# Kernel optimization log

Hardware: AMD Instinct MI355X
Metric: run time of the kernel (lower is better)

The kernel has to match this reference:

```python
import jax, jax.numpy as jnp
import numpy as np
from jax import lax

B, T, D = 4, 4096, 1024
NEG_BIG = -1e30  # stand-in for -inf initial max-state; identical after clamp(min=-30)


def setup_inputs() -> dict:
    key = jax.random.key(0)
    ks = jax.random.split(key, 10)
    x = jax.random.normal(ks[0], (B, T, D), dtype=jnp.float32)
    time_mix_k = jax.random.uniform(ks[1], (D,), dtype=jnp.float32)
    time_mix_v = jax.random.uniform(ks[2], (D,), dtype=jnp.float32)
    time_mix_r = jax.random.uniform(ks[3], (D,), dtype=jnp.float32)
    s = 1.0 / np.sqrt(D)
    W_k = jax.random.normal(ks[4], (D, D), dtype=jnp.float32) * s
    W_v = jax.random.normal(ks[5], (D, D), dtype=jnp.float32) * s
    W_r = jax.random.normal(ks[6], (D, D), dtype=jnp.float32) * s
    W_o = jax.random.normal(ks[7], (D, D), dtype=jnp.float32) * s
    time_decay = -(jax.random.uniform(ks[8], (D,), dtype=jnp.float32) + 0.5)
    time_first = jax.random.normal(ks[9], (D,), dtype=jnp.float32) * 0.1
    return {"x": x, "time_mix_k": time_mix_k, "time_mix_v": time_mix_v,
            "time_mix_r": time_mix_r, "W_k": W_k, "W_v": W_v, "W_r": W_r,
            "W_o": W_o, "time_decay": time_decay, "time_first": time_first}


def _wkv_scan(k, v, w, u):
    # k, v: [B, T, D]; w, u: [D]. Numerically-stable max-subtract WKV scan.
    b, t, d = k.shape
    p0 = jnp.full((b, d), NEG_BIG, dtype=k.dtype)  # running max exponent
    q0 = jnp.zeros((b, d), dtype=k.dtype)          # rescaled numerator state

    def step(carry, kv_t):
        p, q = carry
        k_t, v_t = kv_t
        new_p = jnp.maximum(p, u + k_t)
        scale_old = jnp.exp(jnp.maximum(p - new_p, -30.0))
        scale_cur = jnp.exp(jnp.maximum(u + k_t - new_p, -30.0))
        wkv = (scale_old * q + scale_cur * v_t) / (scale_old + scale_cur + 1e-9)
        new_p2 = jnp.maximum(p + w, k_t)
        scale_prev = jnp.exp(jnp.maximum(p + w - new_p2, -30.0))
        scale_new = jnp.exp(jnp.maximum(k_t - new_p2, -30.0))
        q2 = scale_prev * q + scale_new * v_t
        return (new_p2, q2), wkv

    kT = jnp.swapaxes(k, 0, 1)  # [T, B, D]
    vT = jnp.swapaxes(v, 0, 1)
    _, wkv = lax.scan(step, (p0, q0), (kT, vT))
    return jnp.swapaxes(wkv, 0, 1)  # [B, T, D]


def reference(x, time_mix_k, time_mix_v, time_mix_r, W_k, W_v, W_r, W_o,
              time_decay, time_first):
    # token shift: x_prev[t] = x[t-1], zeros at t=0
    x_prev = jnp.pad(x[:, :-1, :], ((0, 0), (1, 0), (0, 0)))
    xk = x * time_mix_k + x_prev * (1.0 - time_mix_k)
    xv = x * time_mix_v + x_prev * (1.0 - time_mix_v)
    xr = x * time_mix_r + x_prev * (1.0 - time_mix_r)
    # torch nn.Linear (no bias): y = x @ W.T
    k = jnp.einsum('btd,ed->bte', xk, W_k)
    v = jnp.einsum('btd,ed->bte', xv, W_v)
    r = jax.nn.sigmoid(jnp.einsum('btd,ed->bte', xr, W_r))
    wkv = _wkv_scan(k, v, time_decay, time_first)
    y = r * wkv
    return jnp.einsum('btd,ed->bte', y, W_o)
```

## Files before the change

kernel.cpp:

```cpp
#include <hip/hip_runtime.h>
#include <stdint.h>

#define D_DIM 1024
#define T_DIM 4096
#define B_DIM 4
#define M_DIM (B_DIM * T_DIM)
#define NCH 64
#define CHL 64
#define GEMM_N 1024
#define GEMM_K 1024

typedef short bf16x8 __attribute__((ext_vector_type(8)));
typedef float f32x4 __attribute__((ext_vector_type(4)));

__device__ __forceinline__ ushort f2bf(float f) {
    union { float f; uint32_t u; } x; x.f = f;
    uint32_t r = x.u + 0x7fffu + ((x.u >> 16) & 1u);
    return (ushort)(r >> 16);
}
__device__ __forceinline__ float bf2f(ushort u) {
    union { uint32_t u; float f; } x; x.u = (uint32_t)u << 16; return x.f;
}

__device__ __forceinline__ void gload16(const ushort* g, ushort* l) {
    __builtin_amdgcn_global_load_lds(
        (const __attribute__((address_space(1))) void*)g,
        (__attribute__((address_space(3))) void*)l, 16, 0, 0);
}

__global__ void convw(const float* __restrict__ w0, const float* __restrict__ w1,
                      const float* __restrict__ w2, const float* __restrict__ w3,
                      ushort* __restrict__ out) {
    int i = blockIdx.x * 256 + threadIdx.x;
    int sel = i >> 18;
    const float* src = sel == 0 ? w0 : sel == 1 ? w1 : sel == 2 ? w2 : w3;
    int off = (i & 0x3ffff) << 2;
    float4 f = *(const float4*)(src + off);
    ushort4 o; o.x = f2bf(f.x); o.y = f2bf(f.y); o.z = f2bf(f.z); o.w = f2bf(f.w);
    *(ushort4*)(out + (size_t)i * 4) = o;
}

__global__ void mixz(const float* __restrict__ x, const float* __restrict__ tm,
                     ushort* __restrict__ o) {
    size_t gid = (size_t)blockIdx.x * 256 + threadIdx.x;
    size_t e = gid * 4;
    int d = (int)(e & (D_DIM - 1));
    int t = (int)((e >> 10) & (T_DIM - 1));
    float4 xc = *(const float4*)(x + e);
    float4 xp = make_float4(0.f, 0.f, 0.f, 0.f);
    if (t > 0) xp = *(const float4*)(x + e - D_DIM);
    float4 m = *(const float4*)(tm + d);
    ushort4 r;
    r.x = f2bf(xc.x * m.x + xp.x * (1.f - m.x));
    r.y = f2bf(xc.y * m.y + xp.y * (1.f - m.y));
    r.z = f2bf(xc.z * m.z + xp.z * (1.f - m.z));
    r.w = f2bf(xc.w * m.w + xp.w * (1.f - m.w));
    *(ushort4*)(o + e) = r;
}

__global__ void mixall(const float* __restrict__ x,
                       const float* __restrict__ mk, const float* __restrict__ mv,
                       const float* __restrict__ mr,
                       ushort* __restrict__ xk, ushort* __restrict__ xv,
                       ushort* __restrict__ xr) {
    size_t gid = (size_t)blockIdx.x * 256 + threadIdx.x;
    size_t e = gid * 4;
    int d = (int)(e & (D_DIM - 1));
    int t = (int)((e >> 10) & (T_DIM - 1));
    float4 xc = *(const float4*)(x + e);
    float4 xp = make_float4(0.f, 0.f, 0.f, 0.f);
    if (t > 0) xp = *(const float4*)(x + e - D_DIM);
    float4 a = *(const float4*)(mk + d);
    float4 b = *(const float4*)(mv + d);
    float4 c = *(const float4*)(mr + d);
    ushort4 ok, ov, orr;
    ok.x = f2bf(xc.x * a.x + xp.x * (1.f - a.x));
    ok.y = f2bf(xc.y * a.y + xp.y * (1.f - a.y));
    ok.z = f2bf(xc.z * a.z + xp.z * (1.f - a.z));
    ok.w = f2bf(xc.w * a.w + xp.w * (1.f - a.w));
    ov.x = f2bf(xc.x * b.x + xp.x * (1.f - b.x));
    ov.y = f2bf(xc.y * b.y + xp.y * (1.f - b.y));
    ov.z = f2bf(xc.z * b.z + xp.z * (1.f - b.z));
    ov.w = f2bf(xc.w * b.w + xp.w * (1.f - b.w));
    orr.x = f2bf(xc.x * c.x + xp.x * (1.f - c.x));
    orr.y = f2bf(xc.y * c.y + xp.y * (1.f - c.y));
    orr.z = f2bf(xc.z * c.z + xp.z * (1.f - c.z));
    orr.w = f2bf(xc.w * c.w + xp.w * (1.f - c.w));
    *(ushort4*)(xk + e) = ok;
    *(ushort4*)(xv + e) = ov;
    *(ushort4*)(xr + e) = orr;
}

template <int OUTF32>
__global__ void __launch_bounds__(256)
gemm_bt(const ushort* __restrict__ A0, const ushort* __restrict__ B0,
        void* __restrict__ Cv, size_t sA, size_t sB, size_t sC) {
    constexpr int K = GEMM_K, N = GEMM_N;
    __shared__ ushort As[128 * 32];
    __shared__ ushort Bs[128 * 32];
    const int z = blockIdx.z;
    const ushort* A = A0 + (size_t)z * sA;
    const ushort* Bw = B0 + (size_t)z * sB;

    const int id = blockIdx.y * 8 + blockIdx.x;
    const int L = (id & 7) * 128 + (id >> 3);
    const int bx = L & 7, by = L >> 3;

    const int tid = threadIdx.x;
    const int wid = tid >> 6, lane = tid & 63;
    const int wr = wid >> 1, wc = wid & 1;

    const ushort* Ab = A + (size_t)by * 128 * K;
    const ushort* Bb = Bw + (size_t)bx * 128 * K;
    const ushort* ga = Ab + (size_t)(tid >> 2) * K + ((tid & 3) << 3);
    const ushort* gb = Bb + (size_t)(tid >> 2) * K + ((tid & 3) << 3);
    ushort* lA0 = &As[wid * 512];
    ushort* lA1 = &As[2048 + wid * 512];
    ushort* lB0 = &Bs[wid * 512];
    ushort* lB1 = &Bs[2048 + wid * 512];
    const size_t rstep = (size_t)64 * K;

    f32x4 acc[4][4] = {};
    const int frow = lane & 15;
    const int kgrp = (lane >> 4) << 3;

    for (int kt = 0; kt < K; kt += 32) {
        __syncthreads();
        gload16(ga + kt, lA0);
        gload16(ga + kt + rstep, lA1);
        gload16(gb + kt, lB0);
        gload16(gb + kt + rstep, lB1);
        __syncthreads();
        bf16x8 af[4], bfr[4];
#pragma unroll
        for (int m = 0; m < 4; ++m)
            af[m] = *(const bf16x8*)&As[(wr * 64 + m * 16 + frow) * 32 + kgrp];
#pragma unroll
        for (int n = 0; n < 4; ++n)
            bfr[n] = *(const bf16x8*)&Bs[(wc * 64 + n * 16 + frow) * 32 + kgrp];
#pragma unroll
        for (int m = 0; m < 4; ++m)
#pragma unroll
            for (int n = 0; n < 4; ++n)
                acc[m][n] = __builtin_amdgcn_mfma_f32_16x16x32_bf16(
                    af[m], bfr[n], acc[m][n], 0, 0, 0);
    }

    const int rsub = (lane >> 4) << 2;
    if (OUTF32) {
        float* C = (float*)Cv + (size_t)z * sC;
        const int col = bx * 128 + wc * 64 + frow;
        const int row0 = by * 128 + wr * 64 + rsub;
#pragma unroll
        for (int m = 0; m < 4; ++m)
#pragma unroll
            for (int n = 0; n < 4; ++n)
#pragma unroll
                for (int r = 0; r < 4; ++r)
                    C[(size_t)(row0 + m * 16 + r) * N + col + n * 16] = acc[m][n][r];
    } else {
        ushort* C = (ushort*)Cv + (size_t)z * sC;
        ushort* Cs = As;
        const int gRow0 = by * 128, gCol0 = bx * 128;
#pragma unroll
        for (int ch = 0; ch < 4; ++ch) {
            __syncthreads();
            if ((ch >> 1) == wr) {
                const int mb = (ch & 1) << 1;
#pragma unroll
                for (int mm = 0; mm < 2; ++mm)
#pragma unroll
                    for (int n = 0; n < 4; ++n)
#pragma unroll
                        for (int r = 0; r < 4; ++r) {
                            int lr = ((mb + mm) & 1) * 16 + rsub + r;
                            int lc = wc * 64 + n * 16 + frow;
                            Cs[lr * 128 + lc] = f2bf(acc[mb + mm][n][r]);
                        }
            }
            __syncthreads();
            const int lr1 = tid >> 4, lc1 = (tid & 15) << 3;
            size_t g1 = (size_t)(gRow0 + ch * 32 + lr1) * N + gCol0 + lc1;
            size_t g2 = (size_t)(gRow0 + ch * 32 + 16 + lr1) * N + gCol0 + lc1;
            *(bf16x8*)(C + g1) = *(const bf16x8*)&Cs[tid << 3];
            *(bf16x8*)(C + g2) = *(const bf16x8*)&Cs[2048 + (tid << 3)];
        }
    }
}

__global__ void wkv_passA4(const ushort* __restrict__ k, const ushort* __restrict__ v,
                           const float* __restrict__ w_, float* __restrict__ m_arr,
                           float* __restrict__ s_arr) {
    int gid = blockIdx.x * 256 + threadIdx.x;
    int d4 = gid & 255;
    int b = (gid >> 8) & 3;
    int c = gid >> 10;
    float4 w4 = *(const float4*)(w_ + d4 * 4);
    size_t base = ((size_t)(b * T_DIM + c * CHL)) * D_DIM + d4 * 4;
    float m0 = -1e30f, m1 = -1e30f, m2 = -1e30f, m3 = -1e30f;
    float s0 = 0.f, s1 = 0.f, s2 = 0.f, s3 = 0.f;
#pragma unroll 2
    for (int i = 0; i < CHL; ++i) {
        ushort4 k4 = *(const ushort4*)(k + base + (size_t)i * D_DIM);
        ushort4 v4 = *(const ushort4*)(v + base + (size_t)i * D_DIM);
        float cw = (float)(CHL - 1 - i);
        float e0 = bf2f(k4.x) + cw * w4.x, e1 = bf2f(k4.y) + cw * w4.y;
        float e2 = bf2f(k4.z) + cw * w4.z, e3 = bf2f(k4.w) + cw * w4.w;
        float n0 = fmaxf(m0, e0), n1 = fmaxf(m1, e1);
        float n2 = fmaxf(m2, e2), n3 = fmaxf(m3, e3);
        s0 = s0 * __expf(fmaxf(m0 - n0, -30.f)) + __expf(fmaxf(e0 - n0, -30.f)) * bf2f(v4.x);
        s1 = s1 * __expf(fmaxf(m1 - n1, -30.f)) + __expf(fmaxf(e1 - n1, -30.f)) * bf2f(v4.y);
        s2 = s2 * __expf(fmaxf(m2 - n2, -30.f)) + __expf(fmaxf(e2 - n2, -30.f)) * bf2f(v4.z);
        s3 = s3 * __expf(fmaxf(m3 - n3, -30.f)) + __expf(fmaxf(e3 - n3, -30.f)) * bf2f(v4.w);
        m0 = n0; m1 = n1; m2 = n2; m3 = n3;
    }
    int idx = ((c * B_DIM + b) << 10) + d4 * 4;
    *(float4*)(m_arr + idx) = make_float4(m0, m1, m2, m3);
    *(float4*)(s_arr + idx) = make_float4(s0, s1, s2, s3);
}

__global__ void wkv_passB(const float* __restrict__ m_arr, const float* __restrict__ s_arr,
                          const float* __restrict__ w_, float* __restrict__ pin,
                          float* __restrict__ qin) {
    int gid = blockIdx.x * 256 + threadIdx.x;
    int d = gid & 1023;
    int b = gid >> 10;
    float w = w_[d];
    float Lw = (float)CHL * w;
    float p = -1e30f, q = 0.f;
    for (int c = 0; c < NCH; ++c) {
        int idx = ((c * B_DIM + b) << 10) | d;
        pin[idx] = p; qin[idx] = q;
        float mc = m_arr[idx], sc = s_arr[idx];
        float pn = fmaxf(p + Lw, mc);
        q = __expf(fmaxf(p + Lw - pn, -30.f)) * q +
            __expf(fmaxf(mc - pn, -30.f)) * sc;
        p = pn;
    }
}

__global__ void wkv_passC4(const ushort* __restrict__ k, const ushort* __restrict__ v,
                           const ushort* __restrict__ r, const float* __restrict__ w_,
                           const float* __restrict__ u_, const float* __restrict__ pin,
                           const float* __restrict__ qin, ushort* __restrict__ y) {
    int gid = blockIdx.x * 256 + threadIdx.x;
    int d4 = gid & 255;
    int b = (gid >> 8) & 3;
    int c = gid >> 10;
    float4 w4 = *(const float4*)(w_ + d4 * 4);
    float4 u4 = *(const float4*)(u_ + d4 * 4);
    int sidx = ((c * B_DIM + b) << 10) + d4 * 4;
    float4 p4 = *(const float4*)(pin + sidx);
    float4 q4 = *(const float4*)(qin + sidx);
    float p0 = p4.x, p1 = p4.y, p2 = p4.z, p3 = p4.w;
    float q0 = q4.x, q1 = q4.y, q2 = q4.z, q3 = q4.w;
    size_t base = ((size_t)(b * T_DIM + c * CHL)) * D_DIM + d4 * 4;
#pragma unroll 2
    for (int i = 0; i < CHL; ++i) {
        ushort4 k4 = *(const ushort4*)(k + base);
        ushort4 v4 = *(const ushort4*)(v + base);
        ushort4 r4 = *(const ushort4*)(r + base);
        ushort4 o;
#define WKV_CH(P, Q, KK, VV, RR, W, U, OUT)                                   \
        {                                                                     \
            float kk = bf2f(KK), vv = bf2f(VV), rr = bf2f(RR);                \
            float uk = (U) + kk;                                              \
            float np = fmaxf(P, uk);                                          \
            float so = __expf(fmaxf(P - np, -30.f));                          \
            float sc = __expf(fmaxf(uk - np, -30.f));                         \
            float wkv = (so * Q + sc * vv) / (so + sc + 1e-9f);               \
            float np2 = fmaxf(P + (W), kk);                                   \
            float sp = __expf(fmaxf(P + (W) - np2, -30.f));                   \
            float sn = __expf(fmaxf(kk - np2, -30.f));                        \
            Q = sp * Q + sn * vv;                                             \
            P = np2;                                                          \
            float sig = 1.f / (1.f + __expf(-rr));                            \
            OUT = f2bf(sig * wkv);                                            \
        }
        WKV_CH(p0, q0, k4.x, v4.x, r4.x, w4.x, u4.x, o.x)
        WKV_CH(p1, q1, k4.y, v4.y, r4.y, w4.y, u4.y, o.y)
        WKV_CH(p2, q2, k4.z, v4.z, r4.z, w4.z, u4.z, o.z)
        WKV_CH(p3, q3, k4.w, v4.w, r4.w, w4.w, u4.w, o.w)
#undef WKV_CH
        *(ushort4*)(y + base) = o;
        base += D_DIM;
    }
}

extern "C" void kernel_launch(void* const* d_in, const int* in_sizes, int n_in,
                              void* d_out, int out_size, void* d_ws, size_t ws_size,
                              hipStream_t stream) {
    (void)in_sizes; (void)n_in; (void)out_size;
    const float* x  = (const float*)d_in[0];
    const float* mk = (const float*)d_in[1];
    const float* mv = (const float*)d_in[2];
    const float* mr = (const float*)d_in[3];
    const float* Wk = (const float*)d_in[4];
    const float* Wv = (const float*)d_in[5];
    const float* Wr = (const float*)d_in[6];
    const float* Wo = (const float*)d_in[7];
    const float* td = (const float*)d_in[8];
    const float* tf = (const float*)d_in[9];

    const size_t MD = (size_t)M_DIM * D_DIM;
    const size_t DD = (size_t)D_DIM * D_DIM;
    const size_t CHN = (size_t)B_DIM * D_DIM * NCH;

    size_t need_big = (4 * DD + 6 * MD) * 2 + 4 * CHN * 4;
    size_t need_small = (4 * DD + 4 * MD) * 2 + 4 * CHN * 4;
    if (ws_size < need_small) return;

    dim3 g1(8, 128, 1), g3(8, 128, 3);

    if (ws_size >= need_big) {
        ushort* wcat = (ushort*)d_ws;
        ushort* xcat = wcat + 4 * DD;
        ushort* kvr  = xcat + 3 * MD;
        float* m_arr = (float*)(kvr + 3 * MD);
        float* s_arr = m_arr + CHN;
        float* pin   = s_arr + CHN;
        float* qin   = pin + CHN;
        ushort* ybuf = xcat;

        convw<<<4096, 256, 0, stream>>>(Wk, Wv, Wr, Wo, wcat);
        mixall<<<16384, 256, 0, stream>>>(x, mk, mv, mr,
                                          xcat, xcat + MD, xcat + 2 * MD);
        gemm_bt<0><<<g3, 256, 0, stream>>>(xcat, wcat, kvr, MD, DD, MD);
        wkv_passA4<<<256, 256, 0, stream>>>(kvr, kvr + MD, td, m_arr, s_arr);
        wkv_passB<<<16, 256, 0, stream>>>(m_arr, s_arr, td, pin, qin);
        wkv_passC4<<<256, 256, 0, stream>>>(kvr, kvr + MD, kvr + 2 * MD,
                                            td, tf, pin, qin, ybuf);
        gemm_bt<1><<<g1, 256, 0, stream>>>(ybuf, wcat + 3 * DD, d_out, 0, 0, 0);
    } else {
        ushort* wcat = (ushort*)d_ws;
        ushort* kbuf = wcat + 4 * DD;
        ushort* vbuf = kbuf + MD;
        ushort* rbuf = vbuf + MD;
        ushort* xbuf = rbuf + MD;
        float* m_arr = (float*)(xbuf + MD);
        float* s_arr = m_arr + CHN;
        float* pin   = s_arr + CHN;
        float* qin   = pin + CHN;

        convw<<<4096, 256, 0, stream>>>(Wk, Wv, Wr, Wo, wcat);
        mixz<<<16384, 256, 0, stream>>>(x, mk, xbuf);
        gemm_bt<0><<<g1, 256, 0, stream>>>(xbuf, wcat, kbuf, 0, 0, 0);
        mixz<<<16384, 256, 0, stream>>>(x, mv, xbuf);
        gemm_bt<0><<<g1, 256, 0, stream>>>(xbuf, wcat + DD, vbuf, 0, 0, 0);
        mixz<<<16384, 256, 0, stream>>>(x, mr, xbuf);
        gemm_bt<0><<<g1, 256, 0, stream>>>(xbuf, wcat + 2 * DD, rbuf, 0, 0, 0);
        wkv_passA4<<<256, 256, 0, stream>>>(kbuf, vbuf, td, m_arr, s_arr);
        wkv_passB<<<16, 256, 0, stream>>>(m_arr, s_arr, td, pin, qin);
        wkv_passC4<<<256, 256, 0, stream>>>(kbuf, vbuf, rbuf, td, tf, pin, qin, xbuf);
        gemm_bt<1><<<g1, 256, 0, stream>>>(xbuf, wcat + 3 * DD, d_out, 0, 0, 0);
    }
}
```

Baseline: 445.4 us.

## Double-buffer GEMM LDS loads and stage fp32 output through shared memory

Turns the GEMM main loop into a two-stage pipeline. The next K tile's global-to-LDS loads are issued before the current tile's MFMAs, with manual vmcnt waits and raw barriers. The fp32 output path now stages through LDS and writes coalesced float4 rows instead of scattered scalar stores. LDS use doubles to 32KB per block, which may lower occupancy, and the hand-written waitcnt logic relies on each stage issuing exactly four loads.

```diff
diff --git a/kernel.cpp b/kernel.cpp
--- a/kernel.cpp
+++ b/kernel.cpp
@@ -96,8 +96,7 @@
 gemm_bt(const ushort* __restrict__ A0, const ushort* __restrict__ B0,
         void* __restrict__ Cv, size_t sA, size_t sB, size_t sC) {
     constexpr int K = GEMM_K, N = GEMM_N;
-    __shared__ ushort As[128 * 32];
-    __shared__ ushort Bs[128 * 32];
+    __shared__ ushort shm[16384];
     const int z = blockIdx.z;
     const ushort* A = A0 + (size_t)z * sA;
     const ushort* Bw = B0 + (size_t)z * sB;
@@ -114,23 +113,33 @@
     const ushort* Bb = Bw + (size_t)bx * 128 * K;
     const ushort* ga = Ab + (size_t)(tid >> 2) * K + ((tid & 3) << 3);
     const ushort* gb = Bb + (size_t)(tid >> 2) * K + ((tid & 3) << 3);
-    ushort* lA0 = &As[wid * 512];
-    ushort* lA1 = &As[2048 + wid * 512];
-    ushort* lB0 = &Bs[wid * 512];
-    ushort* lB1 = &Bs[2048 + wid * 512];
     const size_t rstep = (size_t)64 * K;
 
     f32x4 acc[4][4] = {};
     const int frow = lane & 15;
     const int kgrp = (lane >> 4) << 3;
 
-    for (int kt = 0; kt < K; kt += 32) {
-        __syncthreads();
-        gload16(ga + kt, lA0);
-        gload16(ga + kt + rstep, lA1);
-        gload16(gb + kt, lB0);
-        gload16(gb + kt + rstep, lB1);
-        __syncthreads();
+    auto stage = [&](int kt, int b) {
+        ushort* la = &shm[b * 4096 + wid * 512];
+        ushort* lb = &shm[8192 + b * 4096 + wid * 512];
+        gload16(ga + kt, la);
+        gload16(ga + kt + rstep, la + 2048);
+        gload16(gb + kt, lb);
+        gload16(gb + kt + rstep, lb + 2048);
+    };
+
+    stage(0, 0);
+    for (int t = 0; t < 32; ++t) {
+        const int cur = t & 1;
+        if (t < 31) {
+            stage((t + 1) << 5, cur ^ 1);
+            asm volatile("s_waitcnt vmcnt(4)" ::: "memory");
+        } else {
+            asm volatile("s_waitcnt vmcnt(0)" ::: "memory");
+        }
+        __builtin_amdgcn_s_barrier();
+        const ushort* As = &shm[cur * 4096];
+        const ushort* Bs = &shm[8192 + cur * 4096];
         bf16x8 af[4], bfr[4];
 #pragma unroll
         for (int m = 0; m < 4; ++m)
@@ -144,24 +153,14 @@
             for (int n = 0; n < 4; ++n)
                 acc[m][n] = __builtin_amdgcn_mfma_f32_16x16x32_bf16(
                     af[m], bfr[n], acc[m][n], 0, 0, 0);
+        __builtin_amdgcn_s_barrier();
     }
 
     const int rsub = (lane >> 4) << 2;
+    const int gRow0 = by * 128, gCol0 = bx * 128;
     if (OUTF32) {
         float* C = (float*)Cv + (size_t)z * sC;
-        const int col = bx * 128 + wc * 64 + frow;
-        const int row0 = by * 128 + wr * 64 + rsub;
-#pragma unroll
-        for (int m = 0; m < 4; ++m)
-#pragma unroll
-            for (int n = 0; n < 4; ++n)
-#pragma unroll
-                for (int r = 0; r < 4; ++r)
-                    C[(size_t)(row0 + m * 16 + r) * N + col + n * 16] = acc[m][n][r];
-    } else {
-        ushort* C = (ushort*)Cv + (size_t)z * sC;
-        ushort* Cs = As;
-        const int gRow0 = by * 128, gCol0 = bx * 128;
+        float* Cs = (float*)shm;
 #pragma unroll
         for (int ch = 0; ch < 4; ++ch) {
             __syncthreads();
@@ -172,11 +171,35 @@
 #pragma unroll
                     for (int n = 0; n < 4; ++n)
 #pragma unroll
-                        for (int r = 0; r < 4; ++r) {
-                            int lr = ((mb + mm) & 1) * 16 + rsub + r;
-                            int lc = wc * 64 + n * 16 + frow;
-                            Cs[lr * 128 + lc] = f2bf(acc[mb + mm][n][r]);
-                        }
+                        for (int r = 0; r < 4; ++r)
+                            Cs[(mm * 16 + rsub + r) * 128 + wc * 64 + n * 16 + frow]
+                                = acc[mb + mm][n][r];
+            }
+            __syncthreads();
+#pragma unroll
+            for (int pass = 0; pass < 4; ++pass) {
+                int lr = pass * 8 + (tid >> 5);
+                int lc = (tid & 31) << 2;
+                *(float4*)(C + (size_t)(gRow0 + ch * 32 + lr) * N + gCol0 + lc)
+                    = *(const float4*)&Cs[lr * 128 + lc];
+            }
+        }
+    } else {
+        ushort* C = (ushort*)Cv + (size_t)z * sC;
+        ushort* Cs = shm;
+#pragma unroll
+        for (int ch = 0; ch < 4; ++ch) {
+            __syncthreads();
+            if ((ch >> 1) == wr) {
+                const int mb = (ch & 1) << 1;
+#pragma unroll
+                for (int mm = 0; mm < 2; ++mm)
+#pragma unroll
+                    for (int n = 0; n < 4; ++n)
+#pragma unroll
+                        for (int r = 0; r < 4; ++r)
+                            Cs[(mm * 16 + rsub + r) * 128 + wc * 64 + n * 16 + frow]
+                                = f2bf(acc[mb + mm][n][r]);
             }
             __syncthreads();
             const int lr1 = tid >> 4, lc1 = (tid & 15) << 3;
```

New measurement: 429.8 us. 1.04x faster.
